# Performance work log

Hardware: AMD Instinct MI355X
Metric: run time of the kernel (lower is better)

Reference implementation:

```python
import jax, jax.numpy as jnp
import numpy as np

EPS = 1e-4  # torch EPS[torch.float32]


def sym_logm(x):
    """Matrix log of symmetric (near-)PD matrices via eigh, eigenvalues clamped at EPS."""
    w, v = jnp.linalg.eigh(x)
    w = jnp.clip(w, EPS)
    return jnp.einsum('...ij,...j,...kj->...ik', v, jnp.log(w), v)


def lower_triangle(x):
    """Vectorize lower triangle; off-diagonal entries scaled by sqrt(2)."""
    n = x.shape[-1]
    r, c = np.tril_indices(n)
    scale = jnp.asarray(np.where(r == c, 1.0, np.sqrt(2.0)), dtype=x.dtype)
    return x[..., r, c] * scale  # [..., n(n+1)/2]


def diff_exp(X, s):
    """Divided-difference derivative of matrix exp at eigenvalues s, applied to X."""
    den = s[:, None] - s[None, :]
    is_eq = jnp.abs(den) < EPS
    den = jnp.where(is_eq, 1.0, den)
    es = jnp.exp(s)
    num = jnp.where(is_eq, 0.5 * (es[:, None] + es[None, :]), es[:, None] - es[None, :])
    return (num / den) * X


def setup_inputs() -> dict:
    key = jax.random.key(0)
    k1, k2, k3 = jax.random.split(key, 3)
    N, M, T, V, C = 32, 2, 64, 25, 16
    out_dims, k = 64, 1
    dim = k + C * (C + 1) // 2  # 137
    # SPD inputs: A A^T / C + 0.5 I
    A = jax.random.normal(k1, (N, M, T, V, C, C), dtype=jnp.float32)
    x = A @ jnp.swapaxes(A, -1, -2) / C + 0.5 * jnp.eye(C, dtype=jnp.float32)
    # W initialized near identity (torch init is eye); small sym perturbation exercises both Diff_Exp branches
    Wn = 0.1 * jax.random.normal(k2, (C, C), dtype=jnp.float32)
    W = jnp.eye(C, dtype=jnp.float32) + 0.5 * (Wn + Wn.T)
    Wb = jax.random.normal(k3, (out_dims, dim), dtype=jnp.float32) / np.sqrt(dim)
    return {"x": x, "W": W, "Wb": Wb}


def reference(x, W, Wb):
    k = 1
    N, M, T, V, C, _ = x.shape
    x = x.reshape(N, -1, C, C)  # [N, MTV, C, C]
    # LEM branch
    W_sym = 0.5 * (W + W.T)
    s = jnp.linalg.svd(W_sym, compute_uv=False)  # [C]
    logx = sym_logm(x)                           # [N, MTV, C, C]
    x_mean = jnp.mean(logx, axis=1, keepdims=True)
    x_center = diff_exp(logx - x_mean, s)
    xc = lower_triangle(x_center)                # [N, MTV, D], D = C(C+1)/2
    x_cov = jnp.einsum('npi,npj->nij', xc, xc) / (T * V * M - 1)  # [N, D, D]
    xm = lower_triangle(sym_logm(x_mean))        # [N, 1, D]
    D = xc.shape[-1]
    chol = jnp.linalg.cholesky(x_cov)
    out = jnp.zeros((N, D + k, D + k), dtype=x.dtype)
    out = out.at[:, :D, :D].set(chol)
    out = out.at[:, D:, :D].set(jnp.broadcast_to(xm, (N, k, D)))
    out = out.at[:, D:, D:].set(jnp.eye(k, dtype=x.dtype))
    tr = jnp.trace(out, axis1=-2, axis2=-1)[:, None, None]
    out = out / tr + tr * jnp.eye(D + k, dtype=x.dtype) * 1e-6
    # BiMap: W_b X W_b^T
    return jnp.einsum('oi,nij,qj->noq', Wb, out, Wb)  # [N, out_dims, out_dims]
```

## Files before the change

### kernel.cpp

```cpp
#include <hip/hip_runtime.h>
#include <math.h>


#define EPSV 1e-4f
#define NSWEEP_BIG 6
#define NSWEEP_SMALL 10
#define SQRT2F 1.41421356237309515f

#define OFF_G      0
#define OFF_WBT    160
#define OFF_MEAN   8960
#define OFF_XM     13312
#define OFF_TR     17664
#define OFF_CT     17792
#define OFF_MPART  320000
#define OFF_PART   320000
#define OFF_L      2704896

typedef float v2f __attribute__((ext_vector_type(2)));

__device__ __forceinline__ float rcp_f(float x){ return __builtin_amdgcn_rcpf(x); }
__device__ __forceinline__ float rsq_f(float x){ return __builtin_amdgcn_rsqf(x); }

__device__ __forceinline__ v2f pk_fma(v2f a, v2f b, v2f c){
    v2f d;
    asm("v_pk_fma_f32 %0, %1, %2, %3" : "=v"(d) : "v"(a), "v"(b), "v"(c));
    return d;
}
__device__ __forceinline__ v2f pk_mul(v2f a, v2f b){
    v2f d;
    asm("v_pk_mul_f32 %0, %1, %2" : "=v"(d) : "v"(a), "v"(b));
    return d;
}

template<int R>
__device__ __forceinline__ float xl(float x){
    int s = __float_as_int(x);
    if constexpr (R == 1){
        return __int_as_float(__builtin_amdgcn_update_dpp(s, s, 0xB1, 0xF, 0xF, false));
    } else if constexpr (R == 2){
        return __int_as_float(__builtin_amdgcn_update_dpp(s, s, 0x4E, 0xF, 0xF, false));
    } else if constexpr (R == 3){
        return __int_as_float(__builtin_amdgcn_update_dpp(s, s, 0x1B, 0xF, 0xF, false));
    } else if constexpr (R == 7){
        return __int_as_float(__builtin_amdgcn_update_dpp(s, s, 0x141, 0xF, 0xF, false));
    } else if constexpr (R == 8){
        return __int_as_float(__builtin_amdgcn_update_dpp(s, s, 0x128, 0xF, 0xF, false));
    } else {
        return __int_as_float(__builtin_amdgcn_update_dpp(s, s, 0x140, 0xF, 0xF, false));
    }
}

template<int R>
__device__ __forceinline__ float shuf(float x){
    if constexpr ((R >= 4 && R <= 6) || R >= 9){
        constexpr int IMM = (R << 10) | 0x1F;
        return __int_as_float(__builtin_amdgcn_ds_swizzle(__float_as_int(x), IMM));
    } else {
        return xl<R>(x);
    }
}

__device__ __forceinline__ void tri_rc(int d, int &r, int &c){
    int rr = (int)floorf((sqrtf(fmaf(8.f, (float)d, 1.f)) - 1.f) * 0.5f);
    if (rr*(rr+1)/2 > d) rr--;
    if ((rr+1)*(rr+2)/2 <= d) rr++;
    r = rr; c = d - rr*(rr+1)/2;
}

template<int R, bool WV>
__device__ __forceinline__ int jac_round(v2f* b, v2f* v, float &nrm, int t){
    v2f pc[8];
#pragma unroll
    for (int i = 0; i < 8; ++i){ pc[i].x = shuf<R>(b[i].x); pc[i].y = shuf<R>(b[i].y); }
    float pn = shuf<R>(nrm);
    v2f ga = pk_mul(b[0], pc[0]);
    v2f gb = pk_mul(b[1], pc[1]);
    ga = pk_fma(b[2], pc[2], ga); gb = pk_fma(b[3], pc[3], gb);
    ga = pk_fma(b[4], pc[4], ga); gb = pk_fma(b[5], pc[5], gb);
    ga = pk_fma(b[6], pc[6], ga); gb = pk_fma(b[7], pc[7], gb);
    float gam = (ga.x + gb.x) + (ga.y + gb.y);
    bool live = (gam*gam > 1.6e-13f * (nrm * pn));
    int lv = __any((int)live);
    if (lv){
        constexpr int HB = (R & 8) ? 8 : ((R & 4) ? 4 : ((R & 2) ? 2 : 1));
        const bool isp = ((t & HB) == 0);
        float d = (nrm - pn) + (isp ? 1e-30f : -1e-30f);
        float g22 = gam + gam;
        float nrr = fmaf(g22, g22, d*d);
        float inv_r = rsq_f(nrr);
        float c2 = fmaf(0.5f*fabsf(d), inv_r, 0.5f);
        float cinv = rsq_f(c2);
        float smag = fabsf(gam) * inv_r * cinv;
        int sgn = (__float_as_int(gam) ^ __float_as_int(d)) & 0x80000000;
        bool zn = (nrr == 0.f);
        float c = zn ? 1.f : c2 * cinv;
        float s = zn ? 0.f : __int_as_float(__float_as_int(smag) | sgn);
        v2f cv = {c, c};
        v2f sv = {s, s};
#pragma unroll
        for (int i = 0; i < 8; ++i) b[i] = pk_fma(pc[i], sv, pk_mul(b[i], cv));
        if (WV){
            v2f pv[8];
#pragma unroll
            for (int i = 0; i < 8; ++i){ pv[i].x = shuf<R>(v[i].x); pv[i].y = shuf<R>(v[i].y); }
#pragma unroll
            for (int i = 0; i < 8; ++i) v[i] = pk_fma(pv[i], sv, pk_mul(v[i], cv));
        }
        nrm = fmaf(s * cinv, gam, nrm);
    }
    return lv;
}

template<bool WV>
__device__ __forceinline__ int jac_sweep(v2f* b, v2f* v, float &nrm, int t){
    int lv = 0;
    lv |= jac_round< 4,WV>(b,v,nrm,t); lv |= jac_round< 1,WV>(b,v,nrm,t);
    lv |= jac_round< 5,WV>(b,v,nrm,t); lv |= jac_round< 2,WV>(b,v,nrm,t);
    lv |= jac_round< 6,WV>(b,v,nrm,t); lv |= jac_round< 3,WV>(b,v,nrm,t);
    lv |= jac_round< 9,WV>(b,v,nrm,t); lv |= jac_round< 7,WV>(b,v,nrm,t);
    lv |= jac_round<10,WV>(b,v,nrm,t); lv |= jac_round< 8,WV>(b,v,nrm,t);
    lv |= jac_round<11,WV>(b,v,nrm,t); lv |= jac_round<15,WV>(b,v,nrm,t);
    lv |= jac_round<12,WV>(b,v,nrm,t); lv |= jac_round<13,WV>(b,v,nrm,t);
    lv |= jac_round<14,WV>(b,v,nrm,t);
    return lv;
}

__global__ __launch_bounds__(256) void k_logm(const float* __restrict__ x,
                                              float* __restrict__ L,
                                              float* __restrict__ mpart,
                                              const float* __restrict__ W,
                                              const float* __restrict__ Wb,
                                              float* __restrict__ ws){
    __shared__ float sm[5120];
    const int tid = threadIdx.x;
    const int t = tid & 15;
    const int g = tid >> 4;
    if (blockIdx.x == 6400){
        float* sigv  = sm;
        float* s_srt = sm + 16;
        if (tid < 64){
            v2f b[8]; float nrm = 0.f;
            float* bf = (float*)b;
#pragma unroll
            for (int i = 0; i < 16; ++i){
                float val = 0.5f * (W[i*16 + t] + W[t*16 + i]);
                bf[i] = val;
                nrm = fmaf(val, val, nrm);
            }
#pragma unroll 1
            for (int sw = 0; sw < NSWEEP_SMALL; ++sw)
                if (!jac_sweep<false>(b, b, nrm, t)) break;
            float n2 = 0.f;
#pragma unroll
            for (int i = 0; i < 16; ++i) n2 = fmaf(bf[i], bf[i], n2);
            float sig = sqrtf(n2);
            if (tid < 16) sigv[t] = sig;
        }
        __syncthreads();
        if (tid < 16){
            float sig = sigv[t];
            int rank = 0;
#pragma unroll
            for (int u = 0; u < 16; ++u){
                float su = sigv[u];
                rank += (su > sig || (su == sig && u < t)) ? 1 : 0;
            }
            s_srt[rank] = sig;
        }
        for (int e = tid; e < 8768; e += 256){
            int o = e / 137, i = e - o*137;
            ws[OFF_WBT + i*64 + o] = Wb[e];
        }
        __syncthreads();
        if (tid < 136){
            int r, c; tri_rc(tid, r, c);
            float sr = s_srt[r], sc = s_srt[c];
            float den = sr - sc;
            bool eq = fabsf(den) < EPSV;
            float er = expf(sr), ec = expf(sc);
            float num = eq ? 0.5f*(er + ec) : (er - ec);
            float dd  = eq ? 1.f : den;
            float scale = (r == c) ? 1.f : SQRT2F;
            ws[OFF_G + tid] = scale * num / dd;
        }
        return;
    }
    float* Bl = sm;
    const size_t m = (size_t)blockIdx.x * 16 + g;
    const float* xp = x + m * 256;
    v2f b[8]; float nrm = 0.f;
    float* bf = (float*)b;
#pragma unroll
    for (int i = 0; i < 16; ++i){
        float val = xp[i*16 + t];
        bf[i] = val;
        nrm = fmaf(val, val, nrm);
    }
#pragma unroll 1
    for (int sw = 0; sw < NSWEEP_BIG; ++sw)
        if (!jac_sweep<false>(b, b, nrm, t)) break;
    float n2 = 0.f;
#pragma unroll
    for (int i = 0; i < 16; ++i) n2 = fmaf(bf[i], bf[i], n2);
    float lam = sqrtf(n2);
    float w = logf(fmaxf(lam, EPSV));
    float coef = w / n2;
#pragma unroll
    for (int i = 0; i < 16; ++i) Bl[g*320 + i*20 + t] = bf[i];
    Bl[g*320 + (t>>2)*20 + 16 + (t&3)] = coef;
    __syncthreads();
    float outv[9];
    float* Lp = L + m * 136;
#pragma unroll
    for (int k = 0; k < 9; ++k){
        int d = t + 16*k;
        float acc = 0.f;
        if (d < 136){
            int r, c; tri_rc(d, r, c);
            const float4* Br = (const float4*)&Bl[g*320 + r*20];
            const float4* Bc = (const float4*)&Bl[g*320 + c*20];
            v2f a2 = {0.f, 0.f};
#pragma unroll
            for (int j4 = 0; j4 < 4; ++j4){
                float4 br = Br[j4], bc = Bc[j4];
                float4 cf = *(const float4*)&Bl[g*320 + j4*20 + 16];
                v2f p1 = pk_mul((v2f){br.x, br.y}, (v2f){cf.x, cf.y});
                a2 = pk_fma(p1, (v2f){bc.x, bc.y}, a2);
                v2f p2 = pk_mul((v2f){br.z, br.w}, (v2f){cf.z, cf.w});
                a2 = pk_fma(p2, (v2f){bc.z, bc.w}, a2);
            }
            acc = a2.x + a2.y;
            Lp[d] = acc;
        }
        outv[k] = acc;
    }
    __syncthreads();
    float* red = sm;
#pragma unroll
    for (int k = 0; k < 9; ++k){
        int d = t + 16*k;
        red[g*144 + d] = outv[k];
    }
    __syncthreads();
    if (tid < 136){
        float s = 0.f;
#pragma unroll
        for (int gg = 0; gg < 16; ++gg) s += red[gg*144 + tid];
        mpart[(size_t)blockIdx.x * 136 + tid] = s;
    }
}

__global__ __launch_bounds__(512) void k_xm_mean(float* __restrict__ ws){
    __shared__ float part[3][136];
    const int n = blockIdx.x;
    const int tid = threadIdx.x;
    const int h = tid / 136;
    const int d = tid - h*136;
    if (tid < 408){
        int c0 = h*67, c1 = (h == 2) ? 200 : (c0 + 67);
        const float* mp = ws + OFF_MPART + (size_t)n * 200 * 136 + d;
        float s = 0.f;
#pragma unroll 4
        for (int c = c0; c < c1; ++c) s += mp[(size_t)c * 136];
        part[h][d] = s;
    }
    __syncthreads();
    if (tid < 136)
        ws[OFF_MEAN + n*136 + tid] =
            ((part[0][tid] + part[1][tid]) + part[2][tid]) * (1.f/3200.f);
}

__global__ __launch_bounds__(256) void k_cov(float* __restrict__ ws){
    __shared__ __align__(16) float xc[16][136];
    __shared__ __align__(16) float Gl[136];
    __shared__ __align__(16) float Ml[136];
    const int bid = blockIdx.x;
    const int tid = threadIdx.x;
    if (bid >= 512){
        const int n = bid - 512;
        float* smf = &xc[0][0];
        float* Ms  = smf;
        float* Vl  = smf + 144;
        float* Hl2 = smf + 464;
        if (tid < 136) Ms[tid] = ws[OFF_MEAN + n*136 + tid];
        __syncthreads();
        const int t = tid & 15;
        if (tid < 64){
            v2f b[8], v[8]; float nrm = 0.f;
            float* bf = (float*)b;
            float* vf = (float*)v;
#pragma unroll
            for (int i = 0; i < 16; ++i){
                int r = (i > t) ? i : t, c = (i > t) ? t : i;
                bf[i] = Ms[r*(r+1)/2 + c];
                vf[i] = (i == t) ? 1.f : 0.f;
                nrm = fmaf(bf[i], bf[i], nrm);
            }
#pragma unroll 1
            for (int sw = 0; sw < NSWEEP_SMALL; ++sw)
                if (!jac_sweep<true>(b, v, nrm, t)) break;
            float lam = 0.f;
#pragma unroll
            for (int i = 0; i < 16; ++i) lam = fmaf(vf[i], bf[i], lam);
            float w = logf(fmaxf(lam, EPSV));
            if (tid < 16){
#pragma unroll
                for (int i = 0; i < 16; ++i){ Vl[i*20 + t] = vf[i]; Hl2[i*20 + t] = w * vf[i]; }
            }
        }
        __syncthreads();
        if (tid < 16){
            for (int k = 0; k < 9; ++k){
                int d = t + 16*k;
                if (d < 136){
                    int r, c; tri_rc(d, r, c);
                    float acc = 0.f;
#pragma unroll
                    for (int j = 0; j < 16; ++j) acc = fmaf(Hl2[r*20 + j], Vl[c*20 + j], acc);
                    float scale = (r == c) ? 1.f : SQRT2F;
                    ws[OFF_XM + n*136 + d] = scale * acc;
                }
            }
        }
        return;
    }
    const int n = bid & 31, c8 = (bid >> 5) & 7, hf = bid >> 8;
    if (tid < 136){
        Gl[tid] = ws[OFF_G + tid];
        Ml[tid] = ws[OFF_MEAN + n*136 + tid];
    }
    int bi = 0, bj = 0; const bool val = (tid < 153);
    if (val){
        int T = hf*153 + tid;
        int bb = (int)floorf((sqrtf(fmaf(4.f, (float)T, 1.f)) - 1.f) * 0.5f);
        while (bb*bb + bb > T) bb--;
        while ((bb+1)*(bb+1) + (bb+1) <= T) bb++;
        bi = bb; bj = T - bb*bb - bb;
    }
    v2f av[16];
#pragma unroll
    for (int i = 0; i < 16; ++i) av[i] = (v2f){0.f, 0.f};
    const float* Lbase = ws + OFF_L + (size_t)n * 3200 * 136;
    for (int st = 0; st < 25; ++st){
        __syncthreads();
        int p0 = c8*400 + st*16;
        for (int f = tid; f < 544; f += 256){
            int pp = f / 34, dd = f - pp*34;
            float4 lv = *(const float4*)(Lbase + (size_t)(p0+pp)*136 + dd*4);
            float4 gv = *(const float4*)(&Gl[dd*4]);
            float4 mv = *(const float4*)(&Ml[dd*4]);
            float4 r;
            r.x = (lv.x - mv.x) * gv.x; r.y = (lv.y - mv.y) * gv.y;
            r.z = (lv.z - mv.z) * gv.z; r.w = (lv.w - mv.w) * gv.w;
            *(float4*)(&xc[pp][dd*4]) = r;
        }
        __syncthreads();
        if (val){
#pragma unroll 1
            for (int pp = 0; pp < 16; ++pp){
                const float4 u0 = *(const float4*)(&xc[pp][bi*8]);
                const float4 u1 = *(const float4*)(&xc[pp][bi*8+4]);
                const float4 w4 = *(const float4*)(&xc[pp][bj*4]);
                v2f u01 = {u0.x, u0.y}, u23 = {u0.z, u0.w};
                v2f u45 = {u1.x, u1.y}, u67 = {u1.z, u1.w};
                float wj[4] = {w4.x, w4.y, w4.z, w4.w};
#pragma unroll
                for (int dj = 0; dj < 4; ++dj){
                    v2f wb = {wj[dj], wj[dj]};
                    av[0*4+dj] = pk_fma(u01, wb, av[0*4+dj]);
                    av[1*4+dj] = pk_fma(u23, wb, av[1*4+dj]);
                    av[2*4+dj] = pk_fma(u45, wb, av[2*4+dj]);
                    av[3*4+dj] = pk_fma(u67, wb, av[3*4+dj]);
                }
            }
        }
    }
    if (val){
        float* part = ws + OFF_PART + ((size_t)c8*32 + n)*9316;
#pragma unroll
        for (int p = 0; p < 4; ++p){
#pragma unroll
            for (int h = 0; h < 2; ++h){
                int i = bi*8 + p*2 + h;
#pragma unroll
                for (int dj = 0; dj < 4; ++dj){
                    int j = bj*4 + dj;
                    if (j <= i) part[i*(i+1)/2 + j] = av[p*4+dj][h];
                }
            }
        }
    }
}

#define TST 141
__global__ __launch_bounds__(512) void k_chol(float* __restrict__ ws){
    __shared__ float T[136*TST];
    __shared__ float dg[136];
    __shared__ float rc2[136];
    const int n = blockIdx.x;
    const int tid = threadIdx.x;
    for (int e = tid; e < 9316; e += 512){
        float s = 0.f;
#pragma unroll
        for (int c = 0; c < 8; ++c) s += ws[OFF_PART + ((size_t)c*32 + n)*9316 + e];
        int r, cc2; tri_rc(e, r, cc2);
        T[r*TST + cc2] = s * (1.f/3199.f);
    }
    __syncthreads();
    for (int k = 0; k < 135; ++k){
        float dkk = sqrtf(T[k*TST + k]);
        float rinv = 1.f / dkk;
        const int m = 135 - k;
        const int cnt = m*(m+1)/2;
        const int Lc = (cnt + 511) >> 9;
        int e0 = tid * Lc, e1 = e0 + Lc; if (e1 > cnt) e1 = cnt;
        if (e0 < e1){
            float A = 2.f*m + 1.f;
            int jp = (int)floorf((A - sqrtf(fmaf(A, A, -8.f*e0))) * 0.5f);
            if (jp < 0) jp = 0;
            while (jp > 0 && jp*m - jp*(jp-1)/2 > e0) jp--;
            while ((jp+1)*m - (jp+1)*jp/2 <= e0) jp++;
            int ip = jp + (e0 - (jp*m - jp*(jp-1)/2));
            int i = k+1+ip, j = k+1+jp;
            int ix = i*TST + j;
            int e = e0;
            while (e < e1){
                int nb = e1 - e; if (nb > 8) nb = 8;
                int   ixs[8]; float cis[8], cjs[8], tv[8];
#pragma unroll
                for (int b2 = 0; b2 < 8; ++b2){
                    if (b2 < nb){
                        ixs[b2] = ix;
                        cis[b2] = T[i*TST + k] * rinv;
                        cjs[b2] = T[j*TST + k] * rinv;
                        i++; ix += TST;
                        if (i == 136){ j++; i = j; ix = i*TST + j; }
                    }
                }
#pragma unroll
                for (int b2 = 0; b2 < 8; ++b2) if (b2 < nb) tv[b2] = T[ixs[b2]];
#pragma unroll
                for (int b2 = 0; b2 < 8; ++b2) if (b2 < nb) tv[b2] = fmaf(-cis[b2], cjs[b2], tv[b2]);
#pragma unroll
                for (int b2 = 0; b2 < 8; ++b2) if (b2 < nb) T[ixs[b2]] = tv[b2];
                e += nb;
            }
        }
        __syncthreads();
    }
    if (tid < 136){
        float d = sqrtf(T[tid*TST + tid]);
        dg[tid] = d;
        rc2[tid] = 1.f / d;
    }
    __syncthreads();
    if (tid == 0){
        float tr = 1.f;
        for (int kk = 0; kk < 136; ++kk) tr += dg[kk];
        ws[OFF_TR + n*2]     = tr;
        ws[OFF_TR + n*2 + 1] = 1.f / tr;
    }
    for (int e = tid; e < 9316; e += 512){
        int r, c; tri_rc(e, r, c);
        float v = (r == c) ? dg[c] : T[r*TST + c] * rc2[c];
        ws[OFF_CT + (size_t)n*9320 + e] = v;
    }
}

__global__ __launch_bounds__(512) void k_tail(float* __restrict__ ws,
                                              const float* __restrict__ Wb,
                                              float* __restrict__ out){
    __shared__ __align__(16) float ct[9320];
    __shared__ __align__(16) float wt8[1120];
    __shared__ __align__(16) float tt8[1120];
    __shared__ float xs[137];
    const int bid = blockIdx.x;
    const int n = bid >> 3, qs = bid & 7;
    const int tid = threadIdx.x;
    const float* ctg = ws + OFF_CT + (size_t)n * 9320;
    for (int e = tid; e < 9316; e += 512) ct[e] = ctg[e];
    for (int e = tid; e < 1096; e += 512){
        int ql = e / 137, j = e - ql*137;
        wt8[ql*140 + j] = ws[OFF_WBT + j*64 + qs*8 + ql];
    }
    if (tid < 137) xs[tid] = (tid < 136) ? ws[OFF_XM + n*136 + tid] : 1.f;
    __syncthreads();
    const float tr  = ws[OFF_TR + n*2];
    const float itr = ws[OFF_TR + n*2 + 1];
    const float c6 = tr * 1e-6f;
    for (int task = tid; task < 1096; task += 512){
        int i = task >> 3, ql = task & 7;
        const float* wq = wt8 + ql*140;
        if (i < 136){
            const float* cr = ct + i*(i+1)/2;
            float acc = 0.f;
            for (int j = 0; j <= i; ++j) acc = fmaf(cr[j], wq[j], acc);
            tt8[ql*140 + i] = fmaf(c6, wq[i], itr * acc);
        } else {
            float acc = wq[136];
            for (int j = 0; j < 136; ++j) acc = fmaf(xs[j], wq[j], acc);
            tt8[ql*140 + 136] = fmaf(c6, wq[136], itr * acc);
        }
    }
    __syncthreads();
    for (int e = tid; e < 8768; e += 512){
        int o = e / 137, i = e - o*137;
        ct[o*140 + i] = Wb[e];
    }
    __syncthreads();
    const int o = tid >> 3, ql = tid & 7;
    const float* wr = ct + o*140;
    const float* tq = tt8 + ql*140;
    float acc = 0.f;
#pragma unroll 1
    for (int i = 0; i < 136; i += 4){
        float4 tv = *(const float4*)(tq + i);
        float4 wv = *(const float4*)(wr + i);
        acc = fmaf(tv.x, wv.x, acc); acc = fmaf(tv.y, wv.y, acc);
        acc = fmaf(tv.z, wv.z, acc); acc = fmaf(tv.w, wv.w, acc);
    }
    acc = fmaf(tq[136], wr[136], acc);
    out[(size_t)n*4096 + o*64 + qs*8 + ql] = acc;
}

extern "C" void kernel_launch(void* const* d_in, const int* in_sizes, int n_in,
                              void* d_out, int out_size, void* d_ws, size_t ws_size,
                              hipStream_t stream){
    const float* x   = (const float*)d_in[0];
    const float* W   = (const float*)d_in[1];
    const float* Wb  = (const float*)d_in[2];
    float* out = (float*)d_out;
    float* ws  = (float*)d_ws;

    k_logm   <<<6401, 256, 0, stream>>>(x, ws + OFF_L, ws + OFF_MPART, W, Wb, ws);
    k_xm_mean<<<  32, 512, 0, stream>>>(ws);
    k_cov    <<< 544, 256, 0, stream>>>(ws);
    k_chol   <<<  32, 512, 0, stream>>>(ws);
    k_tail   <<< 256, 512, 0, stream>>>(ws, Wb, out);
}
```

Measured before the change: 711.9 us.

## Use blocked right-looking Cholesky with panel width 8 in k_chol

```diff
diff --git a/kernel.cpp b/kernel.cpp
--- a/kernel.cpp
+++ b/kernel.cpp
@@ -397,7 +397,6 @@
 __global__ __launch_bounds__(512) void k_chol(float* __restrict__ ws){
     __shared__ float T[136*TST];
     __shared__ float dg[136];
-    __shared__ float rc2[136];
     const int n = blockIdx.x;
     const int tid = threadIdx.x;
     for (int e = tid; e < 9316; e += 512){
@@ -408,53 +407,56 @@
         T[r*TST + cc2] = s * (1.f/3199.f);
     }
     __syncthreads();
-    for (int k = 0; k < 135; ++k){
-        float dkk = sqrtf(T[k*TST + k]);
-        float rinv = 1.f / dkk;
-        const int m = 135 - k;
-        const int cnt = m*(m+1)/2;
-        const int Lc = (cnt + 511) >> 9;
-        int e0 = tid * Lc, e1 = e0 + Lc; if (e1 > cnt) e1 = cnt;
-        if (e0 < e1){
-            float A = 2.f*m + 1.f;
-            int jp = (int)floorf((A - sqrtf(fmaf(A, A, -8.f*e0))) * 0.5f);
-            if (jp < 0) jp = 0;
-            while (jp > 0 && jp*m - jp*(jp-1)/2 > e0) jp--;
-            while ((jp+1)*m - (jp+1)*jp/2 <= e0) jp++;
-            int ip = jp + (e0 - (jp*m - jp*(jp-1)/2));
-            int i = k+1+ip, j = k+1+jp;
-            int ix = i*TST + j;
-            int e = e0;
-            while (e < e1){
-                int nb = e1 - e; if (nb > 8) nb = 8;
-                int   ixs[8]; float cis[8], cjs[8], tv[8];
-#pragma unroll
-                for (int b2 = 0; b2 < 8; ++b2){
-                    if (b2 < nb){
-                        ixs[b2] = ix;
-                        cis[b2] = T[i*TST + k] * rinv;
-                        cjs[b2] = T[j*TST + k] * rinv;
-                        i++; ix += TST;
-                        if (i == 136){ j++; i = j; ix = i*TST + j; }
+    for (int p = 0; p < 17; ++p){
+        const int kb = p*8;
+        for (int c = 0; c < 8; ++c){
+            const int k = kb + c;
+            float rkk = T[k*TST + k];
+            for (int c2 = kb; c2 < k; ++c2){
+                float v = T[k*TST + c2];
+                rkk = fmaf(-v, v, rkk);
+            }
+            float dd = sqrtf(rkk);
+            float rinv = 1.f / dd;
+            int i = k + 1 + tid;
+            if (i <= 135){
+                float raw = T[i*TST + k];
+                for (int c2 = kb; c2 < k; ++c2)
+                    raw = fmaf(-T[i*TST + c2], T[k*TST + c2], raw);
+                T[i*TST + k] = raw * rinv;
+            }
+            if (tid == 0) dg[k] = dd;
+            __syncthreads();
+        }
+        const int kb2 = kb + 8;
+        const int m = 136 - kb2;
+        if (m > 0){
+            const int cnt = m*(m+1)/2;
+            const int Lc = (cnt + 511) >> 9;
+            int e0 = tid*Lc, e1 = e0 + Lc; if (e1 > cnt) e1 = cnt;
+            if (e0 < e1){
+                int r, cj; tri_rc(e0, r, cj);
+                int i = kb2 + r, j = kb2 + cj;
+                float ci[8];
+#pragma unroll
+                for (int c = 0; c < 8; ++c) ci[c] = T[i*TST + kb + c];
+                for (int e = e0; e < e1; ++e){
+                    float tv = T[i*TST + j];
+#pragma unroll
+                    for (int c = 0; c < 8; ++c)
+                        tv = fmaf(-ci[c], T[j*TST + kb + c], tv);
+                    T[i*TST + j] = tv;
+                    ++j;
+                    if (j > i && e + 1 < e1){
+                        ++i; j = kb2;
+#pragma unroll
+                        for (int c = 0; c < 8; ++c) ci[c] = T[i*TST + kb + c];
                     }
                 }
-#pragma unroll
-                for (int b2 = 0; b2 < 8; ++b2) if (b2 < nb) tv[b2] = T[ixs[b2]];
-#pragma unroll
-                for (int b2 = 0; b2 < 8; ++b2) if (b2 < nb) tv[b2] = fmaf(-cis[b2], cjs[b2], tv[b2]);
-#pragma unroll
-                for (int b2 = 0; b2 < 8; ++b2) if (b2 < nb) T[ixs[b2]] = tv[b2];
-                e += nb;
-            }
-        }
-        __syncthreads();
-    }
-    if (tid < 136){
-        float d = sqrtf(T[tid*TST + tid]);
-        dg[tid] = d;
-        rc2[tid] = 1.f / d;
-    }
-    __syncthreads();
+            }
+        }
+        __syncthreads();
+    }
     if (tid == 0){
         float tr = 1.f;
         for (int kk = 0; kk < 136; ++kk) tr += dg[kk];
@@ -463,7 +465,7 @@
     }
     for (int e = tid; e < 9316; e += 512){
         int r, c; tri_rc(e, r, c);
-        float v = (r == c) ? dg[c] : T[r*TST + c] * rc2[c];
+        float v = (r == c) ? dg[c] : T[r*TST + c];
         ws[OFF_CT + (size_t)n*9320 + e] = v;
     }
 }
```

After: 578.5 us. -18.7%, faster.
